# Kernel optimization log

Measured on AMD Instinct MI355X. Metric: run time of the kernel, lower is better.

Reference implementation:

```python
import jax, jax.numpy as jnp
import numpy as np

N_NODES = 100000
N_EDGES = 1600000
IN_CH = 128
HID = 128
EMBED = 256
NUM_GRAPHS = 128


def setup_inputs() -> dict:
    key = jax.random.key(0)
    ks = jax.random.split(key, 12)
    x = jax.random.normal(ks[0], (N_NODES, IN_CH), dtype=jnp.float32)
    edge_index = jax.random.randint(ks[1], (2, N_EDGES), 0, N_NODES, dtype=jnp.int64)
    batch = jnp.sort(jax.random.randint(ks[2], (N_NODES,), 0, NUM_GRAPHS, dtype=jnp.int64))
    s = 0.05
    # conv1 MLP: Linear(in_ch,128) -> ReLU -> Linear(128,128)
    W11 = jax.random.normal(ks[3], (IN_CH, HID), dtype=jnp.float32) * s
    b11 = jnp.zeros((HID,), dtype=jnp.float32)
    W12 = jax.random.normal(ks[4], (HID, HID), dtype=jnp.float32) * s
    b12 = jnp.zeros((HID,), dtype=jnp.float32)
    # conv2 MLP: Linear(128,128) -> ReLU -> Linear(128,embed)
    W21 = jax.random.normal(ks[5], (HID, HID), dtype=jnp.float32) * s
    b21 = jnp.zeros((HID,), dtype=jnp.float32)
    W22 = jax.random.normal(ks[6], (HID, EMBED), dtype=jnp.float32) * s
    b22 = jnp.zeros((EMBED,), dtype=jnp.float32)
    gamma = jnp.ones((EMBED,), dtype=jnp.float32)
    beta = jnp.zeros((EMBED,), dtype=jnp.float32)
    return {"x": x, "edge_index": edge_index, "batch": batch,
            "W11": W11, "b11": b11, "W12": W12, "b12": b12,
            "W21": W21, "b21": b21, "W22": W22, "b22": b22,
            "gamma": gamma, "beta": beta}


def _gin_conv(x, src, dst, W_a, b_a, W_b, b_b):
    # GINConv with eps=0: MLP(x + sum_{j in N(i)} x_j)
    msgs = x[src]                                   # [E, d] gather
    agg = jax.ops.segment_sum(msgs, dst, num_segments=N_NODES)  # scatter-add
    h = x + agg
    h = jax.nn.relu(h @ W_a + b_a)
    return h @ W_b + b_b


def reference(x, edge_index, batch, W11, b11, W12, b12, W21, b21, W22, b22, gamma, beta):
    src, dst = edge_index[0], edge_index[1]
    h = jax.nn.relu(_gin_conv(x, src, dst, W11, b11, W12, b12))   # [N, 128]
    h = jax.nn.relu(_gin_conv(h, src, dst, W21, b21, W22, b22))   # [N, 256]
    # global_mean_pool over graphs
    sums = jax.ops.segment_sum(h, batch, num_segments=NUM_GRAPHS)           # [G, 256]
    counts = jax.ops.segment_sum(jnp.ones((N_NODES,), h.dtype), batch, num_segments=NUM_GRAPHS)
    pooled = sums / jnp.maximum(counts, 1.0)[:, None]
    # LayerNorm over last dim (eps=1e-5 as in torch)
    mu = jnp.mean(pooled, axis=-1, keepdims=True)
    var = jnp.var(pooled, axis=-1, keepdims=True)
    out = (pooled - mu) * jax.lax.rsqrt(var + 1e-5) * gamma + beta
    # Dropout in eval mode: identity
    return out
```

## Files before the change

kernel.cpp:

```cpp
#include <hip/hip_runtime.h>

#define GRAPHS 128
#define CHUNKC 8000

typedef _Float16 f16x8 __attribute__((ext_vector_type(8)));
typedef _Float16 f16x4 __attribute__((ext_vector_type(4)));
typedef _Float16 f16x2 __attribute__((ext_vector_type(2)));
typedef float f32x4 __attribute__((ext_vector_type(4)));

__global__ void k_hist(const int* __restrict__ dst, int* __restrict__ histG,
                       int e, int NB, int NW) {
  __shared__ int h[256];
  int t = threadIdx.x, w = blockIdx.x;
  h[t] = 0; __syncthreads();
  int lo = w * CHUNKC, hi = min(lo + CHUNKC, e);
  for (int i = lo + t; i < hi; i += 256) atomicAdd(&h[dst[i] >> 9], 1);
  __syncthreads();
  if (t < NB) histG[t * NW + w] = h[t];
}

__global__ void k_scanA(const int* __restrict__ in, int* __restrict__ out,
                        int* __restrict__ bsum, int N) {
  __shared__ int s[256];
  int t = threadIdx.x, b = blockIdx.x;
  int base = b * 1024 + t * 4;
  int v[4]; int tot = 0;
#pragma unroll
  for (int j = 0; j < 4; ++j) { int i = base + j; v[j] = (i < N) ? in[i] : 0; tot += v[j]; }
  s[t] = tot; __syncthreads();
  for (int o = 1; o < 256; o <<= 1) {
    int x = (t >= o) ? s[t - o] : 0;
    __syncthreads(); s[t] += x; __syncthreads();
  }
  int run = s[t] - tot;
#pragma unroll
  for (int j = 0; j < 4; ++j) { int i = base + j; if (i < N) out[i] = run; run += v[j]; }
  if (t == 255) bsum[b] = s[255];
}

__global__ void k_scanB(int* bsum, int nb) {
  __shared__ int s[256];
  int t = threadIdx.x;
  int v = (t < nb) ? bsum[t] : 0;
  s[t] = v; __syncthreads();
  for (int o = 1; o < 256; o <<= 1) {
    int x = (t >= o) ? s[t - o] : 0;
    __syncthreads(); s[t] += x; __syncthreads();
  }
  if (t < nb) bsum[t] = s[t] - v;
}

__global__ void k_scanC(int* __restrict__ out, const int* __restrict__ bsum, int N) {
  int i = blockIdx.x * 256 + threadIdx.x;
  if (i < N) out[i] += bsum[i >> 10];
}

__global__ void k_part(const int* __restrict__ src, const int* __restrict__ dst,
                       const int* __restrict__ histG, const int* __restrict__ off,
                       int* __restrict__ part, int e, int NB, int NW) {
  __shared__ int hist[256], lbA[256], lbB[256], stmp[256];
  __shared__ int els[CHUNKC];
  int t = threadIdx.x, w = blockIdx.x;
  int hv = (t < NB) ? histG[t * NW + w] : 0;
  hist[t] = hv; stmp[t] = hv; __syncthreads();
  for (int o = 1; o < 256; o <<= 1) {
    int x = (t >= o) ? stmp[t - o] : 0;
    __syncthreads(); stmp[t] += x; __syncthreads();
  }
  lbA[t] = stmp[t] - hv; lbB[t] = stmp[t] - hv;
  __syncthreads();
  int lo = w * CHUNKC, hi = min(lo + CHUNKC, e);
  for (int i = lo + t; i < hi; i += 256) {
    int d = dst[i];
    int p = atomicAdd(&lbB[d >> 9], 1);
    els[p] = src[i] | ((d & 511) << 17);
  }
  __syncthreads();
  int ln = t & 63, wv = t >> 6;
  for (int b = wv; b < NB; b += 4) {
    int c = hist[b], lb = lbA[b];
    long g = off[b * NW + w];
    for (int j = ln; j < c; j += 64) part[g + j] = els[lb + j];
  }
}

__global__ void k_csrb(const int* __restrict__ part, const int* __restrict__ off,
                       int* __restrict__ ptr, int* __restrict__ csr,
                       int e, int NB, int NW, int n) {
  __shared__ int nh[512], ncur[512], stmp[256];
  int t = threadIdx.x, b = blockIdx.x;
  int s0 = off[b * NW];
  int e0 = (b + 1 < NB) ? off[(b + 1) * NW] : e;
  nh[t] = 0; nh[t + 256] = 0; __syncthreads();
  for (int i = s0 + t; i < e0; i += 256) atomicAdd(&nh[((unsigned)part[i]) >> 17], 1);
  __syncthreads();
  int v0 = nh[2 * t], v1 = nh[2 * t + 1];
  int ps = v0 + v1;
  stmp[t] = ps; __syncthreads();
  for (int o = 1; o < 256; o <<= 1) {
    int x = (t >= o) ? stmp[t - o] : 0;
    __syncthreads(); stmp[t] += x; __syncthreads();
  }
  int base = stmp[t] - ps;
  __syncthreads();
  nh[2 * t] = base;   nh[2 * t + 1] = base + v0;
  ncur[2 * t] = base; ncur[2 * t + 1] = base + v0;
  __syncthreads();
#pragma unroll
  for (int q = 0; q < 2; ++q) {
    int vv = t + q * 256;
    int node = (b << 9) + vv;
    if (node <= n) ptr[node] = s0 + nh[vv];
  }
  for (int i = s0 + t; i < e0; i += 256) {
    int u = part[i];
    int p = atomicAdd(&ncur[((unsigned)u) >> 17], 1);
    csr[s0 + p] = u & 0x1FFFF;
  }
}

__global__ void k_cvt(const float* __restrict__ in, _Float16* __restrict__ out, int total4) {
  int i = blockIdx.x * 256 + threadIdx.x;
  if (i >= total4) return;
  float4 v = ((const float4*)in)[i];
  f16x4 h = { (_Float16)v.x, (_Float16)v.y, (_Float16)v.z, (_Float16)v.w };
  ((f16x4*)out)[i] = h;
}

__global__ void k_agg_h(const _Float16* __restrict__ in, _Float16* __restrict__ out,
                        const int* __restrict__ ptr, const int* __restrict__ csr, int n) {
  int gid = blockIdx.x * 256 + threadIdx.x;
  int node = gid >> 6, lane = gid & 63;
  if (node >= n) return;
  const f16x8* inp = (const f16x8*)in;
  int cb = lane & 15, rg = lane >> 4;
  f16x8 self = inp[(size_t)node * 16 + cb];
  float acc[8];
#pragma unroll
  for (int c = 0; c < 8; ++c) acc[c] = (rg == 0) ? (float)self[c] : 0.f;
  int s = ptr[node], deg = ptr[node + 1] - s;
  for (int seg = 0; seg < deg; seg += 64) {
    int my = (seg + lane < deg) ? csr[s + seg + lane] : n;
    int segn = min(deg - seg, 64);
    for (int b2 = 0; b2 < segn; b2 += 32) {
      int jj[8]; f16x8 w[8];
#pragma unroll
      for (int u = 0; u < 8; ++u) jj[u] = __shfl(my, b2 + u * 4 + rg);
#pragma unroll
      for (int u = 0; u < 8; ++u) w[u] = inp[(size_t)jj[u] * 16 + cb];
#pragma unroll
      for (int u = 0; u < 8; ++u)
#pragma unroll
        for (int c = 0; c < 8; ++c) acc[c] += (float)w[u][c];
    }
  }
#pragma unroll
  for (int c = 0; c < 8; ++c) {
    acc[c] += __shfl_xor(acc[c], 16);
    acc[c] += __shfl_xor(acc[c], 32);
  }
  if (rg == 0) {
    f16x8 r;
#pragma unroll
    for (int c = 0; c < 8; ++c) r[c] = (_Float16)acc[c];
    ((f16x8*)out)[(size_t)node * 16 + cb] = r;
  }
}

__global__ void k_wprep_all(const float* __restrict__ W11, const float* __restrict__ W12,
                            const float* __restrict__ W21, const float* __restrict__ W22,
                            f16x8* __restrict__ f11, f16x8* __restrict__ f12,
                            f16x8* __restrict__ f21, f16x8* __restrict__ f22) {
  int id = blockIdx.x * 256 + threadIdx.x;
  const float* W; f16x8* F; int C, cid, fshift;
  if (id < 2048)       { W = W11; F = f11; C = 128; cid = id;        fshift = 3; }
  else if (id < 4096)  { W = W12; F = f12; C = 128; cid = id - 2048; fshift = 3; }
  else if (id < 6144)  { W = W21; F = f21; C = 128; cid = id - 4096; fshift = 3; }
  else if (id < 10240) { W = W22; F = f22; C = 256; cid = id - 6144; fshift = 4; }
  else return;
  int lane = cid & 63;
  int rest = cid >> 6;
  int fc = rest & ((1 << fshift) - 1);
  int kk = rest >> fshift;
  int cout = fc * 16 + (lane & 15);
  int kb = kk * 32 + (lane >> 4) * 8;
  f16x8 v;
#pragma unroll
  for (int b = 0; b < 8; ++b) v[b] = (_Float16)W[(size_t)(kb + b) * C + cout];
  F[cid] = v;
}

__device__ __forceinline__ f16x8 xpose(f32x4 aE, f32x4 aO, int rg) {
  union U2 { _Float16 h[2]; int i; };
  union U8 { int i[4]; f16x8 v; };
  U2 e01, e23, o01, o23;
  e01.h[0] = (_Float16)aE[0]; e01.h[1] = (_Float16)aE[1];
  e23.h[0] = (_Float16)aE[2]; e23.h[1] = (_Float16)aE[3];
  o01.h[0] = (_Float16)aO[0]; o01.h[1] = (_Float16)aO[1];
  o23.h[0] = (_Float16)aO[2]; o23.h[1] = (_Float16)aO[3];
  int e01x1 = __shfl_xor(e01.i, 16), e01x2 = __shfl_xor(e01.i, 32), e01x3 = __shfl_xor(e01.i, 48);
  int e23x1 = __shfl_xor(e23.i, 16), e23x2 = __shfl_xor(e23.i, 32), e23x3 = __shfl_xor(e23.i, 48);
  int o01x1 = __shfl_xor(o01.i, 16), o01x2 = __shfl_xor(o01.i, 32), o01x3 = __shfl_xor(o01.i, 48);
  int o23x1 = __shfl_xor(o23.i, 16), o23x2 = __shfl_xor(o23.i, 32), o23x3 = __shfl_xor(o23.i, 48);
  U8 r;
  r.i[0] = rg == 0 ? e01.i : rg == 1 ? e01x3 : rg == 2 ? o01x2 : o01x1;
  r.i[1] = rg == 0 ? e23.i : rg == 1 ? e23x3 : rg == 2 ? o23x2 : o23x1;
  r.i[2] = rg == 0 ? e01x1 : rg == 1 ? e01x2 : rg == 2 ? o01x3 : o01.i;
  r.i[3] = rg == 0 ? e23x1 : rg == 1 ? e23x2 : rg == 2 ? o23x3 : o23.i;
  return r.v;
}

__launch_bounds__(256, 3)
__global__ void k_mlp128(const _Float16* __restrict__ in, const f16x8* __restrict__ wfA,
                         const float* __restrict__ bA, const f16x8* __restrict__ wfB,
                         const float* __restrict__ bB, _Float16* __restrict__ out, int n) {
  __shared__ f16x8 wf[2048];
  int t = threadIdx.x;
  int r0 = blockIdx.x * 128;
  int lane = t & 63, w = t >> 6;
  int l16 = lane & 15, rg = lane >> 4;
  int rw = w * 32;
  const f16x8* inp = (const f16x8*)in;
#pragma unroll
  for (int i = 0; i < 8; ++i) wf[t + i * 256] = wfA[t + i * 256];
  int ra0 = r0 + rw + l16;      if (ra0 > n) ra0 = n;
  int ra1 = r0 + rw + 16 + l16; if (ra1 > n) ra1 = n;
  f16x8 xf[2][4];
#pragma unroll
  for (int kk = 0; kk < 4; ++kk) {
    xf[0][kk] = inp[(size_t)ra0 * 16 + kk * 4 + rg];
    xf[1][kk] = inp[(size_t)ra1 * 16 + kk * 4 + rg];
  }
  __syncthreads();
  f32x4 acc[2][8];
#pragma unroll
  for (int rs = 0; rs < 2; ++rs)
#pragma unroll
    for (int fc = 0; fc < 8; ++fc) acc[rs][fc] = (f32x4){0.f, 0.f, 0.f, 0.f};
#pragma unroll
  for (int kk = 0; kk < 4; ++kk)
#pragma unroll
    for (int fc = 0; fc < 8; ++fc) {
      f16x8 a = wf[(kk * 8 + fc) * 64 + lane];
      acc[0][fc] = __builtin_amdgcn_mfma_f32_16x16x32_f16(a, xf[0][kk], acc[0][fc], 0, 0, 0);
      acc[1][fc] = __builtin_amdgcn_mfma_f32_16x16x32_f16(a, xf[1][kk], acc[1][fc], 0, 0, 0);
    }
  f16x8 hf[2][4];
#pragma unroll
  for (int fc = 0; fc < 8; ++fc) {
    float4 bv = *(const float4*)(bA + fc * 16 + rg * 4);
#pragma unroll
    for (int rs = 0; rs < 2; ++rs) {
      acc[rs][fc][0] = fmaxf(acc[rs][fc][0] + bv.x, 0.f);
      acc[rs][fc][1] = fmaxf(acc[rs][fc][1] + bv.y, 0.f);
      acc[rs][fc][2] = fmaxf(acc[rs][fc][2] + bv.z, 0.f);
      acc[rs][fc][3] = fmaxf(acc[rs][fc][3] + bv.w, 0.f);
    }
  }
#pragma unroll
  for (int rs = 0; rs < 2; ++rs)
#pragma unroll
    for (int kk = 0; kk < 4; ++kk)
      hf[rs][kk] = xpose(acc[rs][2 * kk], acc[rs][2 * kk + 1], rg);
  __syncthreads();
#pragma unroll
  for (int i = 0; i < 8; ++i) wf[t + i * 256] = wfB[t + i * 256];
  __syncthreads();
#pragma unroll
  for (int rs = 0; rs < 2; ++rs)
#pragma unroll
    for (int fc = 0; fc < 8; ++fc) acc[rs][fc] = (f32x4){0.f, 0.f, 0.f, 0.f};
#pragma unroll
  for (int kk = 0; kk < 4; ++kk)
#pragma unroll
    for (int fc = 0; fc < 8; ++fc) {
      f16x8 b = wf[(kk * 8 + fc) * 64 + lane];
      acc[0][fc] = __builtin_amdgcn_mfma_f32_16x16x32_f16(b, hf[0][kk], acc[0][fc], 0, 0, 0);
      acc[1][fc] = __builtin_amdgcn_mfma_f32_16x16x32_f16(b, hf[1][kk], acc[1][fc], 0, 0, 0);
    }
#pragma unroll
  for (int fc = 0; fc < 8; ++fc) {
    float4 bv = *(const float4*)(bB + fc * 16 + rg * 4);
#pragma unroll
    for (int rs = 0; rs < 2; ++rs) {
      acc[rs][fc][0] = fmaxf(acc[rs][fc][0] + bv.x, 0.f);
      acc[rs][fc][1] = fmaxf(acc[rs][fc][1] + bv.y, 0.f);
      acc[rs][fc][2] = fmaxf(acc[rs][fc][2] + bv.z, 0.f);
      acc[rs][fc][3] = fmaxf(acc[rs][fc][3] + bv.w, 0.f);
    }
  }
  f16x8* outp = (f16x8*)out;
#pragma unroll
  for (int rs = 0; rs < 2; ++rs) {
    int row = r0 + rw + rs * 16 + l16;
#pragma unroll
    for (int kk = 0; kk < 4; ++kk) {
      f16x8 o = xpose(acc[rs][2 * kk], acc[rs][2 * kk + 1], rg);
      if (row < n) outp[(size_t)row * 16 + kk * 4 + rg] = o;
    }
  }
}

__launch_bounds__(256, 3)
__global__ void k_mlp_pool(const _Float16* __restrict__ in, const f16x8* __restrict__ wfA,
                           const float* __restrict__ bA, const f16x8* __restrict__ wfB,
                           const float* __restrict__ bB, const int* __restrict__ batch,
                           float* __restrict__ pool, int n) {
  __shared__ f16x8 wf[2048];
  __shared__ float pool_l[8 * 256];
  int t = threadIdx.x;
  int r0 = blockIdx.x * 128;
  int lane = t & 63, w = t >> 6;
  int l16 = lane & 15, rg = lane >> 4;
  int rw = w * 32;
  const f16x8* inp = (const f16x8*)in;
#pragma unroll
  for (int j = 0; j < 8; ++j) pool_l[j * 256 + t] = 0.f;
#pragma unroll
  for (int i = 0; i < 8; ++i) wf[t + i * 256] = wfA[t + i * 256];
  int ra0 = r0 + rw + l16;      if (ra0 > n) ra0 = n;
  int ra1 = r0 + rw + 16 + l16; if (ra1 > n) ra1 = n;
  f16x8 xf[2][4];
#pragma unroll
  for (int kk = 0; kk < 4; ++kk) {
    xf[0][kk] = inp[(size_t)ra0 * 16 + kk * 4 + rg];
    xf[1][kk] = inp[(size_t)ra1 * 16 + kk * 4 + rg];
  }
  int g0 = batch[r0];
  int rloc = rw + rg * 4;
  int g4[2][4];
#pragma unroll
  for (int fr = 0; fr < 2; ++fr)
#pragma unroll
    for (int j = 0; j < 4; ++j) {
      int row = r0 + rloc + fr * 16 + j;
      g4[fr][j] = (row < n) ? batch[row] : -1;
    }
  __syncthreads();
  f32x4 acc[2][8];
#pragma unroll
  for (int rs = 0; rs < 2; ++rs)
#pragma unroll
    for (int fc = 0; fc < 8; ++fc) acc[rs][fc] = (f32x4){0.f, 0.f, 0.f, 0.f};
#pragma unroll
  for (int kk = 0; kk < 4; ++kk)
#pragma unroll
    for (int fc = 0; fc < 8; ++fc) {
      f16x8 a = wf[(kk * 8 + fc) * 64 + lane];
      acc[0][fc] = __builtin_amdgcn_mfma_f32_16x16x32_f16(a, xf[0][kk], acc[0][fc], 0, 0, 0);
      acc[1][fc] = __builtin_amdgcn_mfma_f32_16x16x32_f16(a, xf[1][kk], acc[1][fc], 0, 0, 0);
    }
  f16x8 hf[2][4];
#pragma unroll
  for (int fc = 0; fc < 8; ++fc) {
    float4 bv = *(const float4*)(bA + fc * 16 + rg * 4);
#pragma unroll
    for (int rs = 0; rs < 2; ++rs) {
      acc[rs][fc][0] = fmaxf(acc[rs][fc][0] + bv.x, 0.f);
      acc[rs][fc][1] = fmaxf(acc[rs][fc][1] + bv.y, 0.f);
      acc[rs][fc][2] = fmaxf(acc[rs][fc][2] + bv.z, 0.f);
      acc[rs][fc][3] = fmaxf(acc[rs][fc][3] + bv.w, 0.f);
    }
  }
#pragma unroll
  for (int rs = 0; rs < 2; ++rs)
#pragma unroll
    for (int kk = 0; kk < 4; ++kk)
      hf[rs][kk] = xpose(acc[rs][2 * kk], acc[rs][2 * kk + 1], rg);
  for (int h = 0; h < 2; ++h) {
    __syncthreads();
#pragma unroll
    for (int i = 0; i < 8; ++i) {
      int id = t + i * 256;
      int lj = id & 63, fcl = (id >> 6) & 7, kk = id >> 9;
      wf[id] = wfB[(kk * 16 + h * 8 + fcl) * 64 + lj];
    }
    __syncthreads();
#pragma unroll
    for (int rs = 0; rs < 2; ++rs)
#pragma unroll
      for (int fc = 0; fc < 8; ++fc) acc[rs][fc] = (f32x4){0.f, 0.f, 0.f, 0.f};
#pragma unroll
    for (int kk = 0; kk < 4; ++kk)
#pragma unroll
      for (int fc = 0; fc < 8; ++fc) {
        f16x8 b = wf[(kk * 8 + fc) * 64 + lane];
        acc[0][fc] = __builtin_amdgcn_mfma_f32_16x16x32_f16(hf[0][kk], b, acc[0][fc], 0, 0, 0);
        acc[1][fc] = __builtin_amdgcn_mfma_f32_16x16x32_f16(hf[1][kk], b, acc[1][fc], 0, 0, 0);
      }
#pragma unroll
    for (int fc = 0; fc < 8; ++fc) {
      int col = h * 128 + fc * 16 + l16;
      float bv = bB[col];
#pragma unroll
      for (int fr = 0; fr < 2; ++fr) {
        f32x4 a = acc[fr][fc];
        float run = fmaxf(a[0] + bv, 0.f);
#pragma unroll
        for (int j = 1; j < 4; ++j) {
          float v = fmaxf(a[j] + bv, 0.f);
          if (g4[fr][j] == g4[fr][j - 1]) run += v;
          else {
            int g = g4[fr][j - 1];
            if (g >= 0) {
              int d = g - g0;
              if (d >= 0 && d < 8) atomicAdd(&pool_l[d * 256 + col], run);
              else atomicAdd(&pool[g * 256 + col], run);
            }
            run = v;
          }
        }
        int g = g4[fr][3];
        if (g >= 0) {
          int d = g - g0;
          if (d >= 0 && d < 8) atomicAdd(&pool_l[d * 256 + col], run);
          else atomicAdd(&pool[g * 256 + col], run);
        }
      }
    }
  }
  __syncthreads();
#pragma unroll
  for (int j = 0; j < 8; ++j) {
    int idx = j * 256 + t;
    int g = g0 + (idx >> 8), col = idx & 255;
    float v = pool_l[idx];
    if (g < GRAPHS && v != 0.f) atomicAdd(&pool[g * 256 + col], v);
  }
}

__global__ void k_starts(const int* __restrict__ batch, int* __restrict__ starts, int n) {
  int g = threadIdx.x;
  if (g > GRAPHS) return;
  int lo = 0, hi = n;
  while (lo < hi) { int mid = (lo + hi) >> 1; if (batch[mid] < g) lo = mid + 1; else hi = mid; }
  starts[g] = lo;
}

__global__ void k_final(const float* __restrict__ pool, const int* __restrict__ starts,
                        const float* __restrict__ gamma, const float* __restrict__ beta,
                        float* __restrict__ out) {
  __shared__ float2 red[256];
  int g = blockIdx.x, ch = threadIdx.x;
  int cnt = starts[g + 1] - starts[g];
  float p = pool[g * 256 + ch] / fmaxf((float)cnt, 1.f);
  red[ch] = make_float2(p, p * p);
  __syncthreads();
  for (int off = 128; off > 0; off >>= 1) {
    if (ch < off) { red[ch].x += red[ch + off].x; red[ch].y += red[ch + off].y; }
    __syncthreads();
  }
  float mu = red[0].x * (1.f / 256.f);
  float var = red[0].y * (1.f / 256.f) - mu * mu;
  out[g * 256 + ch] = (p - mu) * rsqrtf(var + 1e-5f) * gamma[ch] + beta[ch];
}

extern "C" void kernel_launch(void* const* d_in, const int* in_sizes, int n_in,
                              void* d_out, int out_size, void* d_ws, size_t ws_size,
                              hipStream_t stream) {
  const float* x     = (const float*)d_in[0];
  const int*   ei    = (const int*)d_in[1];
  const int*   batch = (const int*)d_in[2];
  const float* W11 = (const float*)d_in[3];  const float* b11 = (const float*)d_in[4];
  const float* W12 = (const float*)d_in[5];  const float* b12 = (const float*)d_in[6];
  const float* W21 = (const float*)d_in[7];  const float* b21 = (const float*)d_in[8];
  const float* W22 = (const float*)d_in[9];  const float* b22 = (const float*)d_in[10];
  const float* gamma = (const float*)d_in[11];
  const float* beta  = (const float*)d_in[12];
  float* out = (float*)d_out;

  int n = in_sizes[0] / 128;
  int e = in_sizes[1] / 2;
  const int* src = ei;
  const int* dstv = ei + e;

  int NB = (n + 511) >> 9;
  int NW = (e + CHUNKC - 1) / CHUNKC;
  int NS = NB * NW;

  char* ws = (char*)d_ws;
  auto alloc = [&](size_t bytes) { char* p = ws; ws += (bytes + 15) & ~(size_t)15; return p; };
  _Float16* P0 = (_Float16*)alloc((size_t)(n + 1) * 128 * 2);
  _Float16* P1 = (_Float16*)alloc((size_t)(n + 1) * 128 * 2);
  float* pool  = (float*)alloc((size_t)GRAPHS * 256 * 4);
  int* ptr     = (int*)alloc((size_t)(n + 1) * 4);
  int* csr     = (int*)alloc((size_t)e * 4);
  int* part    = (int*)alloc((size_t)e * 4);
  int* histG   = (int*)alloc((size_t)NS * 4);
  int* off     = (int*)alloc((size_t)NS * 4);
  int* bsum    = (int*)alloc(256 * 4);
  int* starts  = (int*)alloc((GRAPHS + 1) * 4);
  f16x8* f11 = (f16x8*)alloc(2048 * 16);
  f16x8* f12 = (f16x8*)alloc(2048 * 16);
  f16x8* f21 = (f16x8*)alloc(2048 * 16);
  f16x8* f22 = (f16x8*)alloc(4096 * 16);

  hipMemsetAsync(pool, 0, (size_t)GRAPHS * 256 * 4, stream);
  hipMemsetAsync(P0 + (size_t)n * 128, 0, 256, stream);
  hipMemsetAsync(P1 + (size_t)n * 128, 0, 256, stream);

  int nbk = (NS + 1023) / 1024;
  k_hist <<<NW, 256, 0, stream>>>(dstv, histG, e, NB, NW);
  k_scanA<<<nbk, 256, 0, stream>>>(histG, off, bsum, NS);
  k_scanB<<<1, 256, 0, stream>>>(bsum, nbk);
  k_scanC<<<(NS + 255) / 256, 256, 0, stream>>>(off, bsum, NS);
  k_part <<<NW, 256, 0, stream>>>(src, dstv, histG, off, part, e, NB, NW);
  k_csrb <<<NB, 256, 0, stream>>>(part, off, ptr, csr, e, NB, NW, n);
  k_starts<<<1, 256, 0, stream>>>(batch, starts, n);
  k_wprep_all<<<40, 256, 0, stream>>>(W11, W12, W21, W22, f11, f12, f21, f22);
  k_cvt<<<(n * 32 + 255) / 256, 256, 0, stream>>>(x, P0, n * 32);

  int mb = (n + 127) / 128;
  int ab = (n * 64 + 255) / 256;

  k_agg_h<<<ab, 256, 0, stream>>>(P0, P1, ptr, csr, n);
  k_mlp128<<<mb, 256, 0, stream>>>(P1, f11, b11, f12, b12, P0, n);
  k_agg_h<<<ab, 256, 0, stream>>>(P0, P1, ptr, csr, n);
  k_mlp_pool<<<mb, 256, 0, stream>>>(P1, f21, b21, f22, b22, batch, pool, n);
  k_final<<<GRAPHS, 256, 0, stream>>>(pool, starts, gamma, beta, out);
}
```

Measured before the change: 309.4 us.

## Merge prep kernels and memsets, fold starts into scan, use fma_mix in aggregation

Fuses the fp32-to-fp16 conversion of x, the weight repacking, the pool zeroing and the sentinel-row zeroing into a single k_prep launch, replacing three memsets and two kernels. The graph-start binary search moves into k_scanB, which removes another launch. The aggregation inner loop now uses inline v_fma_mix_f32 so packed fp16 values accumulate into fp32 without separate conversions. CHUNKC is halved, which doubles the histogram and partition blocks but gives each one less work and a smaller shared-memory footprint.

```diff
diff --git a/kernel.cpp b/kernel.cpp
--- a/kernel.cpp
+++ b/kernel.cpp
@@ -1,12 +1,19 @@
 #include <hip/hip_runtime.h>
 
 #define GRAPHS 128
-#define CHUNKC 8000
+#define CHUNKC 4000
 
 typedef _Float16 f16x8 __attribute__((ext_vector_type(8)));
 typedef _Float16 f16x4 __attribute__((ext_vector_type(4)));
 typedef _Float16 f16x2 __attribute__((ext_vector_type(2)));
 typedef float f32x4 __attribute__((ext_vector_type(4)));
+
+__device__ __forceinline__ void fmix_lo(float& a, int w) {
+  asm("v_fma_mix_f32 %0, %1, 1.0, %0 op_sel:[0,0,0] op_sel_hi:[1,0,0]" : "+v"(a) : "v"(w));
+}
+__device__ __forceinline__ void fmix_hi(float& a, int w) {
+  asm("v_fma_mix_f32 %0, %1, 1.0, %0 op_sel:[1,0,0] op_sel_hi:[1,0,0]" : "+v"(a) : "v"(w));
+}
 
 __global__ void k_hist(const int* __restrict__ dst, int* __restrict__ histG,
                        int e, int NB, int NW) {
@@ -38,7 +45,8 @@
   if (t == 255) bsum[b] = s[255];
 }
 
-__global__ void k_scanB(int* bsum, int nb) {
+__global__ void k_scanB(int* bsum, int nb, const int* __restrict__ batch,
+                        int* __restrict__ starts, int n) {
   __shared__ int s[256];
   int t = threadIdx.x;
   int v = (t < nb) ? bsum[t] : 0;
@@ -48,6 +56,11 @@
     __syncthreads(); s[t] += x; __syncthreads();
   }
   if (t < nb) bsum[t] = s[t] - v;
+  if (t <= GRAPHS) {
+    int lo = 0, hi = n;
+    while (lo < hi) { int mid = (lo + hi) >> 1; if (batch[mid] < t) lo = mid + 1; else hi = mid; }
+    starts[t] = lo;
+  }
 }
 
 __global__ void k_scanC(int* __restrict__ out, const int* __restrict__ bsum, int N) {
@@ -119,12 +132,52 @@
   }
 }
 
-__global__ void k_cvt(const float* __restrict__ in, _Float16* __restrict__ out, int total4) {
-  int i = blockIdx.x * 256 + threadIdx.x;
-  if (i >= total4) return;
-  float4 v = ((const float4*)in)[i];
-  f16x4 h = { (_Float16)v.x, (_Float16)v.y, (_Float16)v.z, (_Float16)v.w };
-  ((f16x4*)out)[i] = h;
+__global__ void k_prep(const float* __restrict__ x, _Float16* __restrict__ P0,
+                       _Float16* __restrict__ P1, int n,
+                       const float* __restrict__ W11, const float* __restrict__ W12,
+                       const float* __restrict__ W21, const float* __restrict__ W22,
+                       f16x8* __restrict__ f11, f16x8* __restrict__ f12,
+                       f16x8* __restrict__ f21, f16x8* __restrict__ f22,
+                       float* __restrict__ pool, int cvtb, int wpb, int poolb) {
+  int b = blockIdx.x, t = threadIdx.x;
+  if (b < cvtb) {
+    int i = b * 256 + t;
+    if (i < n * 32) {
+      float4 v = ((const float4*)x)[i];
+      f16x4 h = { (_Float16)v.x, (_Float16)v.y, (_Float16)v.z, (_Float16)v.w };
+      ((f16x4*)P0)[i] = h;
+    }
+    return;
+  }
+  b -= cvtb;
+  if (b < wpb) {
+    int id = b * 256 + t;
+    const float* W; f16x8* F; int C, cid, fshift;
+    if (id < 2048)       { W = W11; F = f11; C = 128; cid = id;        fshift = 3; }
+    else if (id < 4096)  { W = W12; F = f12; C = 128; cid = id - 2048; fshift = 3; }
+    else if (id < 6144)  { W = W21; F = f21; C = 128; cid = id - 4096; fshift = 3; }
+    else if (id < 10240) { W = W22; F = f22; C = 256; cid = id - 6144; fshift = 4; }
+    else return;
+    int lane = cid & 63;
+    int rest = cid >> 6;
+    int fc = rest & ((1 << fshift) - 1);
+    int kk = rest >> fshift;
+    int cout = fc * 16 + (lane & 15);
+    int kb = kk * 32 + (lane >> 4) * 8;
+    f16x8 v;
+#pragma unroll
+    for (int q = 0; q < 8; ++q) v[q] = (_Float16)W[(size_t)(kb + q) * C + cout];
+    F[cid] = v;
+    return;
+  }
+  b -= wpb;
+  if (b < poolb) {
+    int i = b * 256 + t;
+    if (i < GRAPHS * 256) pool[i] = 0.f;
+    return;
+  }
+  if (t < 128) P0[(size_t)n * 128 + t] = (_Float16)0.f;
+  else P1[(size_t)n * 128 + (t - 128)] = (_Float16)0.f;
 }
 
 __global__ void k_agg_h(const _Float16* __restrict__ in, _Float16* __restrict__ out,
@@ -139,19 +192,23 @@
 #pragma unroll
   for (int c = 0; c < 8; ++c) acc[c] = (rg == 0) ? (float)self[c] : 0.f;
   int s = ptr[node], deg = ptr[node + 1] - s;
+  union W { f16x8 v; int i[4]; };
   for (int seg = 0; seg < deg; seg += 64) {
     int my = (seg + lane < deg) ? csr[s + seg + lane] : n;
     int segn = min(deg - seg, 64);
     for (int b2 = 0; b2 < segn; b2 += 32) {
-      int jj[8]; f16x8 w[8];
+      int jj[8]; W w[8];
 #pragma unroll
       for (int u = 0; u < 8; ++u) jj[u] = __shfl(my, b2 + u * 4 + rg);
 #pragma unroll
-      for (int u = 0; u < 8; ++u) w[u] = inp[(size_t)jj[u] * 16 + cb];
+      for (int u = 0; u < 8; ++u) w[u].v = inp[(size_t)jj[u] * 16 + cb];
 #pragma unroll
       for (int u = 0; u < 8; ++u)
 #pragma unroll
-        for (int c = 0; c < 8; ++c) acc[c] += (float)w[u][c];
+        for (int p = 0; p < 4; ++p) {
+          fmix_lo(acc[2 * p], w[u].i[p]);
+          fmix_hi(acc[2 * p + 1], w[u].i[p]);
+        }
     }
   }
 #pragma unroll
@@ -165,29 +222,6 @@
     for (int c = 0; c < 8; ++c) r[c] = (_Float16)acc[c];
     ((f16x8*)out)[(size_t)node * 16 + cb] = r;
   }
-}
-
-__global__ void k_wprep_all(const float* __restrict__ W11, const float* __restrict__ W12,
-                            const float* __restrict__ W21, const float* __restrict__ W22,
-                            f16x8* __restrict__ f11, f16x8* __restrict__ f12,
-                            f16x8* __restrict__ f21, f16x8* __restrict__ f22) {
-  int id = blockIdx.x * 256 + threadIdx.x;
-  const float* W; f16x8* F; int C, cid, fshift;
-  if (id < 2048)       { W = W11; F = f11; C = 128; cid = id;        fshift = 3; }
-  else if (id < 4096)  { W = W12; F = f12; C = 128; cid = id - 2048; fshift = 3; }
-  else if (id < 6144)  { W = W21; F = f21; C = 128; cid = id - 4096; fshift = 3; }
-  else if (id < 10240) { W = W22; F = f22; C = 256; cid = id - 6144; fshift = 4; }
-  else return;
-  int lane = cid & 63;
-  int rest = cid >> 6;
-  int fc = rest & ((1 << fshift) - 1);
-  int kk = rest >> fshift;
-  int cout = fc * 16 + (lane & 15);
-  int kb = kk * 32 + (lane >> 4) * 8;
-  f16x8 v;
-#pragma unroll
-  for (int b = 0; b < 8; ++b) v[b] = (_Float16)W[(size_t)(kb + b) * C + cout];
-  F[cid] = v;
 }
 
 __device__ __forceinline__ f16x8 xpose(f32x4 aE, f32x4 aO, int rg) {
@@ -429,14 +463,6 @@
   }
 }
 
-__global__ void k_starts(const int* __restrict__ batch, int* __restrict__ starts, int n) {
-  int g = threadIdx.x;
-  if (g > GRAPHS) return;
-  int lo = 0, hi = n;
-  while (lo < hi) { int mid = (lo + hi) >> 1; if (batch[mid] < g) lo = mid + 1; else hi = mid; }
-  starts[g] = lo;
-}
-
 __global__ void k_final(const float* __restrict__ pool, const int* __restrict__ starts,
                         const float* __restrict__ gamma, const float* __restrict__ beta,
                         float* __restrict__ out) {
@@ -495,20 +521,20 @@
   f16x8* f21 = (f16x8*)alloc(2048 * 16);
   f16x8* f22 = (f16x8*)alloc(4096 * 16);
 
-  hipMemsetAsync(pool, 0, (size_t)GRAPHS * 256 * 4, stream);
-  hipMemsetAsync(P0 + (size_t)n * 128, 0, 256, stream);
-  hipMemsetAsync(P1 + (size_t)n * 128, 0, 256, stream);
+  int cvtb = (n * 32 + 255) / 256;
+  int wpb = 40;
+  int poolb = (GRAPHS * 256 + 255) / 256;
+  int prepb = cvtb + wpb + poolb + 1;
 
   int nbk = (NS + 1023) / 1024;
+  k_prep <<<prepb, 256, 0, stream>>>(x, P0, P1, n, W11, W12, W21, W22,
+                                     f11, f12, f21, f22, pool, cvtb, wpb, poolb);
   k_hist <<<NW, 256, 0, stream>>>(dstv, histG, e, NB, NW);
   k_scanA<<<nbk, 256, 0, stream>>>(histG, off, bsum, NS);
-  k_scanB<<<1, 256, 0, stream>>>(bsum, nbk);
+  k_scanB<<<1, 256, 0, stream>>>(bsum, nbk, batch, starts, n);
   k_scanC<<<(NS + 255) / 256, 256, 0, stream>>>(off, bsum, NS);
   k_part <<<NW, 256, 0, stream>>>(src, dstv, histG, off, part, e, NB, NW);
   k_csrb <<<NB, 256, 0, stream>>>(part, off, ptr, csr, e, NB, NW, n);
-  k_starts<<<1, 256, 0, stream>>>(batch, starts, n);
-  k_wprep_all<<<40, 256, 0, stream>>>(W11, W12, W21, W22, f11, f12, f21, f22);
-  k_cvt<<<(n * 32 + 255) / 256, 256, 0, stream>>>(x, P0, n * 32);
 
   int mb = (n + 127) / 128;
   int ab = (n * 64 + 255) / 256;
```

Measured after the change: 282.1 us. 1.1x faster.
